# Optimization experiments

Hardware: AMD Instinct MI355X
Metric: run time of the kernel (lower is better)

Reference implementation:

```python
import jax, jax.numpy as jnp
import numpy as np
import math

B, T, C = 8, 2048, 1024
KEY_SIZE, VALUE_SIZE = 1024, 1024


def setup_inputs() -> dict:
    key = jax.random.key(0)
    ks = jax.random.split(key, 7)
    s = 1.0 / math.sqrt(C)
    return {
        "input": jax.random.normal(ks[0], (B, T, C), dtype=jnp.float32),
        "mask": jnp.ones((B, T, 1), dtype=jnp.float32),
        "Wq": jax.random.uniform(ks[1], (C, KEY_SIZE), jnp.float32, -s, s),
        "bq": jax.random.uniform(ks[2], (KEY_SIZE,), jnp.float32, -s, s),
        "Wk": jax.random.uniform(ks[3], (C, KEY_SIZE), jnp.float32, -s, s),
        "bk": jax.random.uniform(ks[4], (KEY_SIZE,), jnp.float32, -s, s),
        "Wv": jax.random.uniform(ks[5], (C, VALUE_SIZE), jnp.float32, -s, s),
        "bv": jax.random.uniform(ks[6], (VALUE_SIZE,), jnp.float32, -s, s),
    }


def reference(input, mask, Wq, bq, Wk, bk, Wv, bv):
    # QKV projections: [B, T, C] @ [C, K] -> [B, T, K]
    query = input @ Wq + bq
    keys = input @ Wk + bk
    values = input @ Wv + bv
    # scores[b, tq, tk] = query[b, tq, :] . keys[b, tk, :]
    scores = jnp.einsum("bqk,btk->bqt", query, keys) / math.sqrt(KEY_SIZE)
    # NOTE: softmax over the QUERY dimension (axis=1), as in the original (dim=1)
    attn = jax.nn.softmax(scores, axis=1)
    out = jnp.einsum("bqt,btv->bqv", attn, values)
    return out * mask
```

## Files before the change

kernel.cpp:

```cpp
#include <hip/hip_runtime.h>
#include <hip/hip_bf16.h>
#include <cstdint>

typedef __attribute__((ext_vector_type(8))) __bf16 bf16x8;
typedef __attribute__((ext_vector_type(4))) float f32x4;
typedef __attribute__((ext_vector_type(8))) unsigned short u16x8;

static __device__ __forceinline__ unsigned short f2b(float f) {
    union { float f; unsigned u; } v; v.f = f;
    unsigned r = v.u + 0x7fffu + ((v.u >> 16) & 1u);
    return (unsigned short)(r >> 16);
}
static __device__ __forceinline__ float b2f(unsigned short b) {
    union { unsigned u; float f; } v; v.u = ((unsigned)b) << 16;
    return v.f;
}

#define LL16(g, l) __builtin_amdgcn_global_load_lds( \
    (const __attribute__((address_space(1))) void*)(g), \
    (__attribute__((address_space(3))) void*)(l), 16, 0, 0)

__global__ void conv_f32_bf16(const float* __restrict__ in,
                              unsigned short* __restrict__ out, long n8) {
    long i = (long)blockIdx.x * blockDim.x + threadIdx.x;
    if (i >= n8) return;
    const float4* p = (const float4*)in + i * 2;
    float4 a = p[0], b = p[1];
    u16x8 r;
    r[0] = f2b(a.x); r[1] = f2b(a.y); r[2] = f2b(a.z); r[3] = f2b(a.w);
    r[4] = f2b(b.x); r[5] = f2b(b.y); r[6] = f2b(b.z); r[7] = f2b(b.w);
    *(u16x8*)(out + i * 8) = r;
}

__global__ void transpose_w(const float* __restrict__ w0,
                            const float* __restrict__ w1,
                            const float* __restrict__ w2,
                            unsigned short* __restrict__ out) {
    __shared__ float tile[32][33];
    int z = blockIdx.z;
    const float* W = (z == 0) ? w0 : (z == 1) ? w1 : w2;
    int n0 = blockIdx.x * 32, c0 = blockIdx.y * 32;
    int tx = threadIdx.x & 31, ty = threadIdx.x >> 5;
    #pragma unroll
    for (int i = 0; i < 32; i += 8)
        tile[ty + i][tx] = W[(long)(c0 + ty + i) * 1024 + n0 + tx];
    __syncthreads();
    unsigned short* o = out + (long)z * 1024 * 1024;
    #pragma unroll
    for (int i = 0; i < 32; i += 8)
        o[(long)(n0 + ty + i) * 1024 + c0 + tx] = f2b(tile[tx][ty + i]);
}

__global__ void scale_vt(unsigned short* __restrict__ Vt,
                         const float* __restrict__ colsum) {
    long i8 = ((long)blockIdx.x * 256 + threadIdx.x) * 8;
    int b = (int)(i8 >> 21);
    int rem = (int)(i8 & ((1 << 21) - 1));
    int t = rem & 2047;
    const float* cs = colsum + b * 2048 + t;
    u16x8 v = *(const u16x8*)(Vt + i8);
    u16x8 o;
    #pragma unroll
    for (int j = 0; j < 8; ++j) o[j] = f2b(b2f(v[j]) / cs[j]);
    *(u16x8*)(Vt + i8) = o;
}


#define BAR() __builtin_amdgcn_s_barrier()
#define WAIT_LGKM0() do { asm volatile("s_waitcnt lgkmcnt(0)" ::: "memory"); \
                          __builtin_amdgcn_sched_barrier(0); } while (0)
#define WAIT_VM2() asm volatile("s_waitcnt vmcnt(2)" ::: "memory")
#define WAIT_VM0() asm volatile("s_waitcnt vmcnt(0)" ::: "memory")

#define STG_A(buf, h, EOFF) do { \
    LL16(((h) ? sA10 : sA00) + (EOFF), &ldsA[buf][h][dst0]); \
    LL16(((h) ? sA11 : sA01) + (EOFF), &ldsA[buf][h][dst1]); } while (0)
#define STG_B(buf, h, EOFF) do { \
    LL16(((h) ? sB10 : sB00) + (EOFF), &ldsB[buf][h][dst0]); \
    LL16(((h) ? sB11 : sB01) + (EOFF), &ldsB[buf][h][dst1]); } while (0)

#define LDA(d, mh) do { _Pragma("unroll") for (int fi = 0; fi < 4; ++fi) { \
    af[fi][0] = *(const bf16x8*)&ldsA[d][wr][baA0 + (mh) * 4096 + fi * 1024]; \
    af[fi][1] = *(const bf16x8*)&ldsA[d][wr][baA1 + (mh) * 4096 + fi * 1024]; } } while (0)
#define LDB(d, nh) do { _Pragma("unroll") for (int fj = 0; fj < 2; ++fj) { \
    bf[fj][0] = *(const bf16x8*)&ldsB[d][wcH][baB0 + (nh) * 2048 + fj * 1024]; \
    bf[fj][1] = *(const bf16x8*)&ldsB[d][wcH][baB1 + (nh) * 2048 + fj * 1024]; } } while (0)

#define MMA(mh, nh) do { \
    __builtin_amdgcn_s_setprio(1); \
    _Pragma("unroll") for (int fi = 0; fi < 4; ++fi) \
    _Pragma("unroll") for (int fj = 0; fj < 2; ++fj) { \
        acc[(mh)*4+fi][(nh)*2+fj] = __builtin_amdgcn_mfma_f32_16x16x32_bf16( \
            af[fi][0], bf[fj][0], acc[(mh)*4+fi][(nh)*2+fj], 0, 0, 0); \
        acc[(mh)*4+fi][(nh)*2+fj] = __builtin_amdgcn_mfma_f32_16x16x32_bf16( \
            af[fi][1], bf[fj][1], acc[(mh)*4+fi][(nh)*2+fj], 0, 0, 0); } \
    __builtin_amdgcn_s_setprio(0); } while (0)

template<int MODE>
__global__ __launch_bounds__(512, 2)
void gemm256(const unsigned short* __restrict__ Aall,
             const unsigned short* __restrict__ Ball,
             void* __restrict__ Cv,
             int M, int N, int K, int ldc,
             long aStride, long bStride, long cStride,
             const float* __restrict__ aux, float* __restrict__ colsum) {
    __shared__ unsigned short ldsA[2][2][8192];
    __shared__ unsigned short ldsB[2][2][8192];

    const int gx = gridDim.x, gy = gridDim.y;
    const int nxy = gx * gy;
    const int nwg = nxy * gridDim.z;
    const int orig = (blockIdx.z * gy + blockIdx.y) * gx + blockIdx.x;
    const int swz = (orig & 7) * (nwg >> 3) + (orig >> 3);
    const int bz = swz / nxy;
    const int rem = swz - bz * nxy;
    const int by = rem / gx;
    const int bx = rem - by * gx;

    const unsigned short* A  = Aall + (long)bz * aStride;
    const unsigned short* Bt = Ball + (long)bz * bStride;

    const int tid = threadIdx.x;
    const int lane = tid & 63;
    const int w = tid >> 6;
    const int wr = w >> 2, wc = w & 3;
    const int wcH = wc >> 1;
    const int lr = lane & 15, lg = lane >> 4;

    const int bm = by * 256, bn = bx * 256;
    const int NI = K >> 7;

    const int r0 = tid >> 3;
    const int l0 = (tid & 7) ^ (r0 & 7);
    const unsigned short* sA00 = A  + (long)(bm + r0)       * K + l0 * 8;
    const unsigned short* sA01 = A  + (long)(bm + 64 + r0)  * K + l0 * 8;
    const unsigned short* sA10 = A  + (long)(bm + 128 + r0) * K + l0 * 8;
    const unsigned short* sA11 = A  + (long)(bm + 192 + r0) * K + l0 * 8;
    const unsigned short* sB00 = Bt + (long)(bn + r0)       * K + l0 * 8;
    const unsigned short* sB01 = Bt + (long)(bn + 64 + r0)  * K + l0 * 8;
    const unsigned short* sB10 = Bt + (long)(bn + 128 + r0) * K + l0 * 8;
    const unsigned short* sB11 = Bt + (long)(bn + 192 + r0) * K + l0 * 8;
    const int dst0 = w * 512;
    const int dst1 = 4096 + w * 512;

    const int cx0 = (lg ^ (lr & 7)) * 8;
    const int cx1 = ((4 + lg) ^ (lr & 7)) * 8;
    const int baA0 = lr * 64 + cx0;
    const int baA1 = lr * 64 + cx1;
    const int baB0 = ((wc & 1) * 64 + lr) * 64 + cx0;
    const int baB1 = ((wc & 1) * 64 + lr) * 64 + cx1;

    bf16x8 af[4][2], bf[2][2];
    f32x4 acc[8][4] = {};

    STG_B(0, 0, 0); STG_B(0, 1, 0); STG_A(0, 0, 0); STG_A(0, 1, 0);
    STG_B(1, 0, 64);
    WAIT_VM2();
    BAR();

    for (int i = 0; i < NI; ++i) {
        const bool more = (i + 1 < NI);
        LDA(0, 0); LDB(0, 0); STG_B(1, 1, 64);
        BAR(); WAIT_LGKM0(); MMA(0, 0); BAR();

        LDA(0, 1); STG_A(1, 0, 64);
        BAR(); WAIT_LGKM0(); MMA(1, 0); BAR();

        LDB(0, 1); STG_A(1, 1, 64);
        BAR(); WAIT_LGKM0(); MMA(1, 1); BAR();

        LDA(0, 0); if (more) STG_B(0, 0, 128);
        BAR(); WAIT_LGKM0(); MMA(0, 1);
        if (more) { WAIT_VM2(); } else { WAIT_VM0(); }
        BAR();

        LDA(1, 0); LDB(1, 0); if (more) STG_B(0, 1, 128);
        BAR(); WAIT_LGKM0(); MMA(0, 0); BAR();

        LDA(1, 1); if (more) STG_A(0, 0, 128);
        BAR(); WAIT_LGKM0(); MMA(1, 0); BAR();

        LDB(1, 1); if (more) STG_A(0, 1, 128);
        BAR(); WAIT_LGKM0(); MMA(1, 1); BAR();

        LDA(1, 0); if (more) STG_B(1, 0, 192);
        BAR(); WAIT_LGKM0(); MMA(0, 1);
        WAIT_VM2();
        BAR();

        sA00 += 128; sA01 += 128; sA10 += 128; sA11 += 128;
        sB00 += 128; sB01 += 128; sB10 += 128; sB11 += 128;
    }

    const int row0 = bm + wr * 128;
    const int col0 = bn + wc * 64;

    if (MODE == 0) {
        unsigned short* C = (unsigned short*)Cv + (long)bz * cStride;
        #pragma unroll
        for (int nj = 0; nj < 4; ++nj) {
            int col = col0 + nj * 16 + lr;
            float bias = aux[col];
            #pragma unroll
            for (int mi = 0; mi < 8; ++mi) {
                int row = row0 + mi * 16 + lg * 4;
                #pragma unroll
                for (int r = 0; r < 4; ++r)
                    C[(long)(row + r) * ldc + col] = f2b(acc[mi][nj][r] + bias);
            }
        }
    } else if (MODE == 1) {
        unsigned short* C = (unsigned short*)Cv + (long)bz * cStride;
        #pragma unroll
        for (int mi = 0; mi < 8; ++mi) {
            #pragma unroll
            for (int r = 0; r < 4; ++r) {
                int row = row0 + mi * 16 + lg * 4 + r;
                float bias = aux[row];
                #pragma unroll
                for (int nj = 0; nj < 4; ++nj) {
                    int col = col0 + nj * 16 + lr;
                    C[(long)row * ldc + col] = f2b(acc[mi][nj][r] + bias);
                }
            }
        }
    } else if (MODE == 2) {
        unsigned short* C = (unsigned short*)Cv + (long)bz * cStride;
        float* cs = colsum + (long)bz * 2048;
        #pragma unroll
        for (int nj = 0; nj < 4; ++nj) {
            int col = col0 + nj * 16 + lr;
            float psum = 0.f;
            #pragma unroll
            for (int mi = 0; mi < 8; ++mi) {
                int row = row0 + mi * 16 + lg * 4;
                #pragma unroll
                for (int r = 0; r < 4; ++r) {
                    float e = __expf(acc[mi][nj][r] * 0.03125f);
                    psum += e;
                    C[(long)(row + r) * ldc + col] = f2b(e);
                }
            }
            psum += __shfl_xor(psum, 16);
            psum += __shfl_xor(psum, 32);
            if (lg == 0) atomicAdd(&cs[col], psum);
        }
    } else {
        float* C = (float*)Cv + (long)bz * cStride;
        const float* mk = aux + (long)bz * 2048;
        #pragma unroll
        for (int mi = 0; mi < 8; ++mi) {
            #pragma unroll
            for (int r = 0; r < 4; ++r) {
                int row = row0 + mi * 16 + lg * 4 + r;
                float m = mk[row];
                #pragma unroll
                for (int nj = 0; nj < 4; ++nj) {
                    int col = col0 + nj * 16 + lr;
                    C[(long)row * ldc + col] = acc[mi][nj][r] * m;
                }
            }
        }
    }
}

extern "C" void kernel_launch(void* const* d_in, const int* in_sizes, int n_in,
                              void* d_out, int out_size, void* d_ws, size_t ws_size,
                              hipStream_t stream) {
    const float* x    = (const float*)d_in[0];
    const float* mask = (const float*)d_in[1];
    const float* Wq   = (const float*)d_in[2];
    const float* bq   = (const float*)d_in[3];
    const float* Wk   = (const float*)d_in[4];
    const float* bk   = (const float*)d_in[5];
    const float* Wv   = (const float*)d_in[6];
    const float* bv   = (const float*)d_in[7];
    float* out = (float*)d_out;

    const long MT = 16384;
    unsigned short* Xb = (unsigned short*)d_ws;
    unsigned short* Wt = Xb + MT * 1024;
    unsigned short* Q  = Wt + 3L * 1024 * 1024;
    unsigned short* Kk = Q  + MT * 1024;
    unsigned short* Vt = Kk + MT * 1024;
    unsigned short* E  = Vt + 8L * 1024 * 2048;
    float* colsum = (float*)(E + 8L * 2048 * 2048);
    size_t need = (size_t)((char*)(colsum + 8 * 2048) - (char*)d_ws);
    if (ws_size < need) return;

    conv_f32_bf16<<<(MT * 1024) / 8 / 256, 256, 0, stream>>>(x, Xb, (MT * 1024) / 8);
    transpose_w<<<dim3(32, 32, 3), 256, 0, stream>>>(Wq, Wk, Wv, Wt);
    gemm256<0><<<dim3(4, 64, 1), 512, 0, stream>>>(
        Xb, Wt, Q, 16384, 1024, 1024, 1024, 0, 0, 0, bq, nullptr);
    gemm256<0><<<dim3(4, 64, 1), 512, 0, stream>>>(
        Xb, Wt + 1048576, Kk, 16384, 1024, 1024, 1024, 0, 0, 0, bk, nullptr);
    gemm256<1><<<dim3(8, 4, 8), 512, 0, stream>>>(
        Wt + 2097152, Xb, Vt, 1024, 2048, 1024, 2048,
        0, 2048L * 1024, 1024L * 2048, bv, nullptr);
    hipMemsetAsync(colsum, 0, 8 * 2048 * sizeof(float), stream);
    gemm256<2><<<dim3(8, 8, 8), 512, 0, stream>>>(
        Q, Kk, E, 2048, 2048, 1024, 2048,
        2048L * 1024, 2048L * 1024, 2048L * 2048, nullptr, colsum);
    scale_vt<<<8192, 256, 0, stream>>>(Vt, colsum);
    gemm256<3><<<dim3(4, 8, 8), 512, 0, stream>>>(
        E, Vt, out, 2048, 1024, 2048, 1024,
        2048L * 2048, 1024L * 2048, 2048L * 1024, mask, nullptr);
}
```

Before: 330.1 us.

## Stage GEMM epilogues through swizzled LDS and reorder MMA quadrants to reuse B fragments

The GEMM epilogue now writes accumulator tiles into LDS with an XOR swizzle and then stores full rows with 16-byte vector writes. The old epilogue did scattered 2-byte or 4-byte global stores. Inside the main loop, the quadrant order is changed so two B-fragment register sets are kept, which removes one redundant LDA reload per half-iteration. The cost is extra barriers, LDS traffic in the epilogue, and more registers, which could hurt occupancy at launch bounds (512,2).

New measurement: 302.1 us. 1.09x faster.

```diff
diff --git a/kernel.cpp b/kernel.cpp
--- a/kernel.cpp
+++ b/kernel.cpp
@@ -67,33 +67,34 @@
 
 
 #define BAR() __builtin_amdgcn_s_barrier()
+#define SCHED0() __builtin_amdgcn_sched_barrier(0)
 #define WAIT_LGKM0() do { asm volatile("s_waitcnt lgkmcnt(0)" ::: "memory"); \
                           __builtin_amdgcn_sched_barrier(0); } while (0)
 #define WAIT_VM2() asm volatile("s_waitcnt vmcnt(2)" ::: "memory")
 #define WAIT_VM0() asm volatile("s_waitcnt vmcnt(0)" ::: "memory")
 
 #define STG_A(buf, h, EOFF) do { \
-    LL16(((h) ? sA10 : sA00) + (EOFF), &ldsA[buf][h][dst0]); \
-    LL16(((h) ? sA11 : sA01) + (EOFF), &ldsA[buf][h][dst1]); } while (0)
+    LL16(((h) ? sA10 : sA00) + (EOFF), ldsA + (buf)*16384 + (h)*8192 + dst0); \
+    LL16(((h) ? sA11 : sA01) + (EOFF), ldsA + (buf)*16384 + (h)*8192 + dst1); } while (0)
 #define STG_B(buf, h, EOFF) do { \
-    LL16(((h) ? sB10 : sB00) + (EOFF), &ldsB[buf][h][dst0]); \
-    LL16(((h) ? sB11 : sB01) + (EOFF), &ldsB[buf][h][dst1]); } while (0)
+    LL16(((h) ? sB10 : sB00) + (EOFF), ldsB + (buf)*16384 + (h)*8192 + dst0); \
+    LL16(((h) ? sB11 : sB01) + (EOFF), ldsB + (buf)*16384 + (h)*8192 + dst1); } while (0)
 
 #define LDA(d, mh) do { _Pragma("unroll") for (int fi = 0; fi < 4; ++fi) { \
-    af[fi][0] = *(const bf16x8*)&ldsA[d][wr][baA0 + (mh) * 4096 + fi * 1024]; \
-    af[fi][1] = *(const bf16x8*)&ldsA[d][wr][baA1 + (mh) * 4096 + fi * 1024]; } } while (0)
-#define LDB(d, nh) do { _Pragma("unroll") for (int fj = 0; fj < 2; ++fj) { \
-    bf[fj][0] = *(const bf16x8*)&ldsB[d][wcH][baB0 + (nh) * 2048 + fj * 1024]; \
-    bf[fj][1] = *(const bf16x8*)&ldsB[d][wcH][baB1 + (nh) * 2048 + fj * 1024]; } } while (0)
-
-#define MMA(mh, nh) do { \
+    af[fi][0] = *(const bf16x8*)(ldsA + (d)*16384 + wr*8192 + baA0 + (mh)*4096 + fi*1024); \
+    af[fi][1] = *(const bf16x8*)(ldsA + (d)*16384 + wr*8192 + baA1 + (mh)*4096 + fi*1024); } } while (0)
+#define LDB(d, nh, BF) do { _Pragma("unroll") for (int fj = 0; fj < 2; ++fj) { \
+    BF[fj][0] = *(const bf16x8*)(ldsB + (d)*16384 + wcH*8192 + baB0 + (nh)*2048 + fj*1024); \
+    BF[fj][1] = *(const bf16x8*)(ldsB + (d)*16384 + wcH*8192 + baB1 + (nh)*2048 + fj*1024); } } while (0)
+
+#define MMA(mh, nh, BF) do { \
     __builtin_amdgcn_s_setprio(1); \
     _Pragma("unroll") for (int fi = 0; fi < 4; ++fi) \
     _Pragma("unroll") for (int fj = 0; fj < 2; ++fj) { \
         acc[(mh)*4+fi][(nh)*2+fj] = __builtin_amdgcn_mfma_f32_16x16x32_bf16( \
-            af[fi][0], bf[fj][0], acc[(mh)*4+fi][(nh)*2+fj], 0, 0, 0); \
+            af[fi][0], BF[fj][0], acc[(mh)*4+fi][(nh)*2+fj], 0, 0, 0); \
         acc[(mh)*4+fi][(nh)*2+fj] = __builtin_amdgcn_mfma_f32_16x16x32_bf16( \
-            af[fi][1], bf[fj][1], acc[(mh)*4+fi][(nh)*2+fj], 0, 0, 0); } \
+            af[fi][1], BF[fj][1], acc[(mh)*4+fi][(nh)*2+fj], 0, 0, 0); } \
     __builtin_amdgcn_s_setprio(0); } while (0)
 
 template<int MODE>
@@ -104,8 +105,9 @@
              int M, int N, int K, int ldc,
              long aStride, long bStride, long cStride,
              const float* __restrict__ aux, float* __restrict__ colsum) {
-    __shared__ unsigned short ldsA[2][2][8192];
-    __shared__ unsigned short ldsB[2][2][8192];
+    __shared__ unsigned short lds[65536];
+    unsigned short* const ldsA = lds;
+    unsigned short* const ldsB = lds + 32768;
 
     const int gx = gridDim.x, gy = gridDim.y;
     const int nxy = gx * gy;
@@ -150,7 +152,7 @@
     const int baB0 = ((wc & 1) * 64 + lr) * 64 + cx0;
     const int baB1 = ((wc & 1) * 64 + lr) * 64 + cx1;
 
-    bf16x8 af[4][2], bf[2][2];
+    bf16x8 af[4][2], bfA[2][2], bfB[2][2];
     f32x4 acc[8][4] = {};
 
     STG_B(0, 0, 0); STG_B(0, 1, 0); STG_A(0, 0, 0); STG_A(0, 1, 0);
@@ -160,31 +162,31 @@
 
     for (int i = 0; i < NI; ++i) {
         const bool more = (i + 1 < NI);
-        LDA(0, 0); LDB(0, 0); STG_B(1, 1, 64);
-        BAR(); WAIT_LGKM0(); MMA(0, 0); BAR();
-
-        LDA(0, 1); STG_A(1, 0, 64);
-        BAR(); WAIT_LGKM0(); MMA(1, 0); BAR();
-
-        LDB(0, 1); STG_A(1, 1, 64);
-        BAR(); WAIT_LGKM0(); MMA(1, 1); BAR();
-
-        LDA(0, 0); if (more) STG_B(0, 0, 128);
-        BAR(); WAIT_LGKM0(); MMA(0, 1);
+        LDA(0, 0); LDB(0, 0, bfA); STG_B(1, 1, 64);
+        BAR(); WAIT_LGKM0(); MMA(0, 0, bfA); BAR();
+
+        LDB(0, 1, bfB); STG_A(1, 0, 64);
+        BAR(); WAIT_LGKM0(); MMA(0, 1, bfB); BAR();
+
+        LDA(0, 1); STG_A(1, 1, 64);
+        BAR(); WAIT_LGKM0(); MMA(1, 1, bfB); BAR();
+
+        if (more) STG_B(0, 0, 128);
+        BAR(); SCHED0(); MMA(1, 0, bfA);
         if (more) { WAIT_VM2(); } else { WAIT_VM0(); }
         BAR();
 
-        LDA(1, 0); LDB(1, 0); if (more) STG_B(0, 1, 128);
-        BAR(); WAIT_LGKM0(); MMA(0, 0); BAR();
-
-        LDA(1, 1); if (more) STG_A(0, 0, 128);
-        BAR(); WAIT_LGKM0(); MMA(1, 0); BAR();
-
-        LDB(1, 1); if (more) STG_A(0, 1, 128);
-        BAR(); WAIT_LGKM0(); MMA(1, 1); BAR();
-
-        LDA(1, 0); if (more) STG_B(1, 0, 192);
-        BAR(); WAIT_LGKM0(); MMA(0, 1);
+        LDA(1, 0); LDB(1, 0, bfA); if (more) STG_B(0, 1, 128);
+        BAR(); WAIT_LGKM0(); MMA(0, 0, bfA); BAR();
+
+        LDB(1, 1, bfB); if (more) STG_A(0, 0, 128);
+        BAR(); WAIT_LGKM0(); MMA(0, 1, bfB); BAR();
+
+        LDA(1, 1); if (more) STG_A(0, 1, 128);
+        BAR(); WAIT_LGKM0(); MMA(1, 1, bfB); BAR();
+
+        if (more) STG_B(1, 0, 192);
+        BAR(); SCHED0(); MMA(1, 0, bfA);
         WAIT_VM2();
         BAR();
 
@@ -192,73 +194,78 @@
         sB00 += 128; sB01 += 128; sB10 += 128; sB11 += 128;
     }
 
-    const int row0 = bm + wr * 128;
-    const int col0 = bn + wc * 64;
-
-    if (MODE == 0) {
-        unsigned short* C = (unsigned short*)Cv + (long)bz * cStride;
-        #pragma unroll
-        for (int nj = 0; nj < 4; ++nj) {
-            int col = col0 + nj * 16 + lr;
-            float bias = aux[col];
-            #pragma unroll
-            for (int mi = 0; mi < 8; ++mi) {
-                int row = row0 + mi * 16 + lg * 4;
-                #pragma unroll
-                for (int r = 0; r < 4; ++r)
-                    C[(long)(row + r) * ldc + col] = f2b(acc[mi][nj][r] + bias);
-            }
-        }
-    } else if (MODE == 1) {
-        unsigned short* C = (unsigned short*)Cv + (long)bz * cStride;
-        #pragma unroll
-        for (int mi = 0; mi < 8; ++mi) {
-            #pragma unroll
-            for (int r = 0; r < 4; ++r) {
-                int row = row0 + mi * 16 + lg * 4 + r;
-                float bias = aux[row];
-                #pragma unroll
-                for (int nj = 0; nj < 4; ++nj) {
-                    int col = col0 + nj * 16 + lr;
-                    C[(long)row * ldc + col] = f2b(acc[mi][nj][r] + bias);
-                }
-            }
-        }
-    } else if (MODE == 2) {
+    const int rloc0 = wr * 128;
+    const int cloc0 = wc * 64;
+
+    if (MODE != 3) {
         unsigned short* C = (unsigned short*)Cv + (long)bz * cStride;
         float* cs = colsum + (long)bz * 2048;
         #pragma unroll
         for (int nj = 0; nj < 4; ++nj) {
-            int col = col0 + nj * 16 + lr;
+            int cl = cloc0 + nj * 16 + lr;
+            int cb = cl >> 3, cIn = cl & 7;
+            float colB = (MODE == 0) ? aux[bn + cl] : 0.f;
             float psum = 0.f;
             #pragma unroll
             for (int mi = 0; mi < 8; ++mi) {
-                int row = row0 + mi * 16 + lg * 4;
                 #pragma unroll
                 for (int r = 0; r < 4; ++r) {
-                    float e = __expf(acc[mi][nj][r] * 0.03125f);
-                    psum += e;
-                    C[(long)(row + r) * ldc + col] = f2b(e);
+                    int rl = rloc0 + mi * 16 + lg * 4 + r;
+                    float v = acc[mi][nj][r];
+                    if (MODE == 0) v += colB;
+                    else if (MODE == 1) v += aux[bm + rl];
+                    else { v = __expf(v * 0.03125f); psum += v; }
+                    int ch = cb ^ ((rl & 7) << 2);
+                    lds[rl * 256 + ch * 8 + cIn] = f2b(v);
                 }
             }
-            psum += __shfl_xor(psum, 16);
-            psum += __shfl_xor(psum, 32);
-            if (lg == 0) atomicAdd(&cs[col], psum);
+            if (MODE == 2) {
+                psum += __shfl_xor(psum, 16);
+                psum += __shfl_xor(psum, 32);
+                if (lg == 0) atomicAdd(&cs[bn + cl], psum);
+            }
+        }
+        BAR();
+        #pragma unroll
+        for (int it = 0; it < 16; ++it) {
+            int lin = it * 512 + tid;
+            int row = lin >> 5;
+            int c = lin & 31;
+            u16x8 v = *(const u16x8*)&lds[row * 256 + ((c ^ ((row & 7) << 2)) << 3)];
+            *(u16x8*)&C[(long)(bm + row) * ldc + bn + c * 8] = v;
         }
     } else {
         float* C = (float*)Cv + (long)bz * cStride;
         const float* mk = aux + (long)bz * 2048;
+        float* ft = (float*)lds;
         #pragma unroll
-        for (int mi = 0; mi < 8; ++mi) {
-            #pragma unroll
-            for (int r = 0; r < 4; ++r) {
-                int row = row0 + mi * 16 + lg * 4 + r;
-                float m = mk[row];
+        for (int h = 0; h < 2; ++h) {
+            if (h) BAR();
+            if (wr == h) {
                 #pragma unroll
                 for (int nj = 0; nj < 4; ++nj) {
-                    int col = col0 + nj * 16 + lr;
-                    C[(long)row * ldc + col] = acc[mi][nj][r] * m;
+                    int cl = cloc0 + nj * 16 + lr;
+                    int cf = cl >> 2, cIn = cl & 3;
+                    #pragma unroll
+                    for (int mi = 0; mi < 8; ++mi) {
+                        #pragma unroll
+                        for (int r = 0; r < 4; ++r) {
+                            int rl = mi * 16 + lg * 4 + r;
+                            float m = mk[bm + h * 128 + rl];
+                            int cfs = cf ^ ((rl & 7) << 2);
+                            ft[rl * 256 + cfs * 4 + cIn] = acc[mi][nj][r] * m;
+                        }
+                    }
                 }
+            }
+            BAR();
+            #pragma unroll
+            for (int it = 0; it < 16; ++it) {
+                int lin = it * 512 + tid;
+                int row = lin >> 6;
+                int cf = lin & 63;
+                float4 v = *(const float4*)&ft[row * 256 + ((cf ^ ((row & 7) << 2)) << 2)];
+                *(float4*)&C[(long)(bm + h * 128 + row) * ldc + bn + cf * 4] = v;
             }
         }
     }
```
